# Performance work log

Hardware: AMD Instinct MI355X
Metric: run time of the kernel (lower is better)

## Reference

```python
import jax, jax.numpy as jnp
import numpy as np

B, T, C = 4, 2048, 1024
H = 16
D = C // H  # 64


def setup_inputs() -> dict:
    key = jax.random.key(0)
    ks = jax.random.split(key, 3)
    scale = 1.0 / np.sqrt(C)
    return {
        "x": jax.random.normal(ks[0], (B, T, C), dtype=jnp.float32),
        "W_attn": jax.random.normal(ks[1], (C, 3 * C), dtype=jnp.float32) * scale,
        "b_attn": jnp.zeros((3 * C,), dtype=jnp.float32),
        "W_proj": jax.random.normal(ks[2], (C, C), dtype=jnp.float32) * scale,
        "b_proj": jnp.zeros((C,), dtype=jnp.float32),
    }


def reference(x, W_attn, b_attn, W_proj, b_proj):
    b, t, c = x.shape
    qkv = x @ W_attn + b_attn                      # [B,T,3C]
    q, k, v = jnp.split(qkv, 3, axis=-1)           # each [B,T,C]
    to_heads = lambda z: z.reshape(b, t, H, D).transpose(0, 2, 1, 3)  # [B,H,T,D]
    q, k, v = to_heads(q), to_heads(k), to_heads(v)
    scores = jnp.einsum("bhtd,bhsd->bhts", q, k) / jnp.sqrt(jnp.float32(D))
    causal = jnp.tril(jnp.ones((t, t), dtype=bool))  # [T,T]
    scores = jnp.where(causal[None, None], scores, jnp.finfo(scores.dtype).min)
    attn = jax.nn.softmax(scores, axis=-1)           # [B,H,T,T]
    out = jnp.einsum("bhts,bhsd->bhtd", attn, v)     # [B,H,T,D]
    out = out.transpose(0, 2, 1, 3).reshape(b, t, c)
    return out @ W_proj + b_proj
```

## Files before the change

### kernel.cpp

```cpp
#include <hip/hip_runtime.h>
#include <hip/hip_bf16.h>

typedef __bf16 bf16_t;
typedef __attribute__((ext_vector_type(8))) __bf16 bf16x8;
typedef __attribute__((ext_vector_type(4))) float f32x4;
typedef __attribute__((ext_vector_type(4))) unsigned short u16x4;
typedef __attribute__((ext_vector_type(4))) unsigned int u32x4;

#define B_DIM 4
#define T_DIM 2048
#define C_DIM 1024
#define H_DIM 16
#define D_DIM 64
#define M_TOK (B_DIM * T_DIM)
#define N_QKV (3 * C_DIM)
#define NT    (T_DIM / 64)
#define KSTR  72
#define CSC   0.18033688011112042f

__device__ __forceinline__ void gload_lds16(const bf16_t* g, bf16_t* l) {
  __builtin_amdgcn_global_load_lds((const __attribute__((address_space(1))) void*)(g),
                                   (__attribute__((address_space(3))) void*)(l), 16, 0, 0);
}

__global__ void cvt_f32_to_bf16(const float* __restrict__ in, bf16_t* __restrict__ out, int n4) {
  int i = blockIdx.x * blockDim.x + threadIdx.x;
  if (i >= n4) return;
  float4 v = ((const float4*)in)[i];
  struct alignas(8) bv4 { bf16_t x, y, z, w; };
  bv4 o;
  o.x = (bf16_t)v.x; o.y = (bf16_t)v.y; o.z = (bf16_t)v.z; o.w = (bf16_t)v.w;
  ((bv4*)out)[i] = o;
}

__global__ void transpose_f32_to_bf16(const float* __restrict__ in, bf16_t* __restrict__ out,
                                      int K, int N) {
  __shared__ float tile[32][33];
  int bx = blockIdx.x * 32;
  int by = blockIdx.y * 32;
  int tx = threadIdx.x, ty = threadIdx.y;
#pragma unroll
  for (int i = 0; i < 32; i += 8)
    tile[ty + i][tx] = in[(size_t)(by + ty + i) * N + bx + tx];
  __syncthreads();
#pragma unroll
  for (int i = 0; i < 32; i += 8)
    out[(size_t)(bx + ty + i) * K + by + tx] = (bf16_t)tile[tx][ty + i];
}

#define BM 128
#define BN 128
#define BK 32

__global__ __launch_bounds__(256, 4)
void gemm_bt_bias(const bf16_t* __restrict__ A, const bf16_t* __restrict__ Bt,
                  const float* __restrict__ bias, bf16_t* __restrict__ Cb,
                  int M, int N, int K) {
  __shared__ alignas(16) bf16_t As[BM * BK];
  __shared__ alignas(16) bf16_t Bs[BN * BK];
  const int tid = threadIdx.x;
  const int lane = tid & 63;
  const int wave = tid >> 6;
  const int wr = (wave >> 1) * 64, wc = (wave & 1) * 64;
  const int quad = lane >> 4, l16 = lane & 15;
  const int row0 = blockIdx.x * BM, col0 = blockIdx.y * BN;

  const int srow = wave * 32 + (lane >> 2);
  const int scol = (lane & 3) * 8;
  const bf16_t* Ag = A + (size_t)(row0 + srow) * K + scol;
  const bf16_t* Bg = Bt + (size_t)(col0 + srow) * K + scol;
  bf16_t* AsW = &As[(wave * 32) * BK];
  bf16_t* BsW = &Bs[(wave * 32) * BK];

  f32x4 acc[4][4];
#pragma unroll
  for (int i = 0; i < 4; ++i)
#pragma unroll
    for (int j = 0; j < 4; ++j)
      acc[i][j] = (f32x4){0.f, 0.f, 0.f, 0.f};

  for (int k0 = 0; k0 < K; k0 += BK) {
    __syncthreads();
    gload_lds16(Ag + k0, AsW);
    gload_lds16(Ag + k0 + (size_t)16 * K, AsW + 16 * BK);
    gload_lds16(Bg + k0, BsW);
    gload_lds16(Bg + k0 + (size_t)16 * K, BsW + 16 * BK);
    __syncthreads();
    bf16x8 af[4], bfr[4];
#pragma unroll
    for (int i = 0; i < 4; ++i)
      af[i] = *(const bf16x8*)&As[(wr + i * 16 + l16) * BK + quad * 8];
#pragma unroll
    for (int j = 0; j < 4; ++j)
      bfr[j] = *(const bf16x8*)&Bs[(wc + j * 16 + l16) * BK + quad * 8];
#pragma unroll
    for (int i = 0; i < 4; ++i)
#pragma unroll
      for (int j = 0; j < 4; ++j)
        acc[i][j] = __builtin_amdgcn_mfma_f32_16x16x32_bf16(af[i], bfr[j], acc[i][j], 0, 0, 0);
  }

#pragma unroll
  for (int i = 0; i < 4; ++i)
#pragma unroll
    for (int j = 0; j < 4; ++j) {
      int col = col0 + wc + j * 16 + l16;
      float bv = bias[col];
#pragma unroll
      for (int r = 0; r < 4; ++r) {
        int row = row0 + wr + i * 16 + quad * 4 + r;
        Cb[(size_t)row * N + col] = (bf16_t)(acc[i][j][r] + bv);
      }
    }
}

__global__ __launch_bounds__(256, 4)
void gemm_bt_bias_n64(const bf16_t* __restrict__ A, const bf16_t* __restrict__ Bt,
                      const float* __restrict__ bias, float* __restrict__ Cf,
                      int M, int N, int K) {
  __shared__ alignas(16) bf16_t As[BM * BK];
  __shared__ alignas(16) bf16_t Bs[64 * BK];
  const int tid = threadIdx.x;
  const int lane = tid & 63;
  const int wave = tid >> 6;
  const int wr = (wave >> 1) * 64, wc = (wave & 1) * 32;
  const int quad = lane >> 4, l16 = lane & 15;
  const int row0 = blockIdx.x * BM, col0 = blockIdx.y * 64;

  const int sr = lane >> 2;
  const int scol = (lane & 3) * 8;
  const bf16_t* Ag = A + (size_t)(row0 + wave * 32 + sr) * K + scol;
  const bf16_t* Bg = Bt + (size_t)(col0 + wave * 16 + sr) * K + scol;
  bf16_t* AsW = &As[(wave * 32) * BK];
  bf16_t* BsW = &Bs[(wave * 16) * BK];

  f32x4 acc[4][2];
#pragma unroll
  for (int i = 0; i < 4; ++i)
#pragma unroll
    for (int j = 0; j < 2; ++j)
      acc[i][j] = (f32x4){0.f, 0.f, 0.f, 0.f};

  for (int k0 = 0; k0 < K; k0 += BK) {
    __syncthreads();
    gload_lds16(Ag + k0, AsW);
    gload_lds16(Ag + k0 + (size_t)16 * K, AsW + 16 * BK);
    gload_lds16(Bg + k0, BsW);
    __syncthreads();
    bf16x8 af[4], bfr[2];
#pragma unroll
    for (int i = 0; i < 4; ++i)
      af[i] = *(const bf16x8*)&As[(wr + i * 16 + l16) * BK + quad * 8];
#pragma unroll
    for (int j = 0; j < 2; ++j)
      bfr[j] = *(const bf16x8*)&Bs[(wc + j * 16 + l16) * BK + quad * 8];
#pragma unroll
    for (int i = 0; i < 4; ++i)
#pragma unroll
      for (int j = 0; j < 2; ++j)
        acc[i][j] = __builtin_amdgcn_mfma_f32_16x16x32_bf16(af[i], bfr[j], acc[i][j], 0, 0, 0);
  }

#pragma unroll
  for (int i = 0; i < 4; ++i)
#pragma unroll
    for (int j = 0; j < 2; ++j) {
      int col = col0 + wc + j * 16 + l16;
      float bv = bias[col];
#pragma unroll
      for (int r = 0; r < 4; ++r) {
        int row = row0 + wr + i * 16 + quad * 4 + r;
        Cf[(size_t)row * N + col] = acc[i][j][r] + bv;
      }
    }
}

__global__ __launch_bounds__(256, 4)
void attn_fwd(const bf16_t* __restrict__ qkv, bf16_t* __restrict__ out) {
  __shared__ alignas(16) bf16_t Ks[64 * KSTR];
  __shared__ alignas(16) bf16_t Vt[64 * KSTR];

  const int tid = threadIdx.x;
  const int lane = tid & 63;
  const int wave = tid >> 6;
  const int quad = lane >> 4, l16 = lane & 15;
  const int qlo = blockIdx.x;
  const int qhi = NT - 1 - qlo;
  const int h = blockIdx.y, b = blockIdx.z;
  const size_t tokBase = (size_t)b * T_DIM;

  const bf16_t* qpl = qkv + (tokBase + qlo * 64 + wave * 16 + l16) * N_QKV + h * D_DIM;
  const bf16_t* qph = qkv + (tokBase + qhi * 64 + wave * 16 + l16) * N_QKV + h * D_DIM;
  bf16x8 ql0 = *(const bf16x8*)(qpl + quad * 8);
  bf16x8 ql1 = *(const bf16x8*)(qpl + 32 + quad * 8);
  bf16x8 qh0 = *(const bf16x8*)(qph + quad * 8);
  bf16x8 qh1 = *(const bf16x8*)(qph + 32 + quad * 8);

  f32x4 ol[4], oh[4];
#pragma unroll
  for (int dt = 0; dt < 4; ++dt) {
    ol[dt] = (f32x4){0.f, 0.f, 0.f, 0.f};
    oh[dt] = (f32x4){0.f, 0.f, 0.f, 0.f};
  }
  float ll = 0.f, lh = 0.f;

  const int tx = tid & 15, ty = tid >> 4;
  const int vswz = ((tx >> 2) & 3) * 8;
  const int vcol = (8 * (ty & 3) + 4 * ((ty >> 2) & 1) + 32 * (ty >> 3)) ^ vswz;
  const f32x4 zero4 = (f32x4){0.f, 0.f, 0.f, 0.f};

  u16x4 kreg[4], vreg[4];
  const bf16_t* kb0 = qkv + (tokBase + ty * 4) * N_QKV + h * D_DIM + C_DIM + tx * 4;
#pragma unroll
  for (int r = 0; r < 4; ++r) kreg[r] = *(const u16x4*)(kb0 + (size_t)r * N_QKV);
#pragma unroll
  for (int r = 0; r < 4; ++r) vreg[r] = *(const u16x4*)(kb0 + (size_t)r * N_QKV + C_DIM);

  for (int t = 0; t <= qhi; ++t) {
    const bool lo = (t <= qlo);
    __syncthreads();
#pragma unroll
    for (int r = 0; r < 4; ++r)
      *(u16x4*)&Ks[(ty * 4 + r) * KSTR + tx * 4] = kreg[r];
#pragma unroll
    for (int i = 0; i < 4; ++i) {
      u16x4 p = (u16x4){vreg[0][i], vreg[1][i], vreg[2][i], vreg[3][i]};
      *(u16x4*)&Vt[(tx * 4 + i) * KSTR + vcol] = p;
    }
    __syncthreads();
    if (t < qhi) {
      const bf16_t* kb = qkv + (tokBase + (t + 1) * 64 + ty * 4) * N_QKV + h * D_DIM + C_DIM + tx * 4;
#pragma unroll
      for (int r = 0; r < 4; ++r) kreg[r] = *(const u16x4*)(kb + (size_t)r * N_QKV);
#pragma unroll
      for (int r = 0; r < 4; ++r) vreg[r] = *(const u16x4*)(kb + (size_t)r * N_QKV + C_DIM);
    }

    f32x4 svl[4], svh[4];
#pragma unroll
    for (int ct = 0; ct < 4; ++ct) {
      bf16x8 kf0 = *(const bf16x8*)&Ks[(ct * 16 + l16) * KSTR + quad * 8];
      bf16x8 kf1 = *(const bf16x8*)&Ks[(ct * 16 + l16) * KSTR + 32 + quad * 8];
      if (lo) {
        svl[ct] = __builtin_amdgcn_mfma_f32_16x16x32_bf16(kf0, ql0, zero4, 0, 0, 0);
        svl[ct] = __builtin_amdgcn_mfma_f32_16x16x32_bf16(kf1, ql1, svl[ct], 0, 0, 0);
      }
      svh[ct] = __builtin_amdgcn_mfma_f32_16x16x32_bf16(kf0, qh0, zero4, 0, 0, 0);
      svh[ct] = __builtin_amdgcn_mfma_f32_16x16x32_bf16(kf1, qh1, svh[ct], 0, 0, 0);
    }
    if (t == qlo) {
      const int qr = wave * 16 + l16;
#pragma unroll
      for (int ct = 0; ct < 4; ++ct)
#pragma unroll
        for (int r = 0; r < 4; ++r)
          if (ct * 16 + quad * 4 + r > qr) svl[ct][r] = -INFINITY;
    }
    if (t == qhi) {
      const int qr = wave * 16 + l16;
#pragma unroll
      for (int ct = 0; ct < 4; ++ct)
#pragma unroll
        for (int r = 0; r < 4; ++r)
          if (ct * 16 + quad * 4 + r > qr) svh[ct][r] = -INFINITY;
    }

    struct alignas(4) bpair { bf16_t lo, hi; };
    bf16x8 pl0, pl1, ph0, ph1;
    if (lo) {
      float rsum = 0.f;
      unsigned int lw[8];
#pragma unroll
      for (int ct = 0; ct < 4; ++ct) {
        float e0 = __builtin_amdgcn_exp2f(svl[ct][0] * CSC);
        float e1 = __builtin_amdgcn_exp2f(svl[ct][1] * CSC);
        float e2 = __builtin_amdgcn_exp2f(svl[ct][2] * CSC);
        float e3 = __builtin_amdgcn_exp2f(svl[ct][3] * CSC);
        rsum += (e0 + e1) + (e2 + e3);
        bpair w0 = {(bf16_t)e0, (bf16_t)e1};
        bpair w1 = {(bf16_t)e2, (bf16_t)e3};
        lw[ct * 2 + 0] = __builtin_bit_cast(unsigned int, w0);
        lw[ct * 2 + 1] = __builtin_bit_cast(unsigned int, w1);
      }
      rsum += __shfl_xor(rsum, 16);
      rsum += __shfl_xor(rsum, 32);
      ll += rsum;
      u32x4 pw0 = (u32x4){lw[0], lw[1], lw[2], lw[3]};
      u32x4 pw1 = (u32x4){lw[4], lw[5], lw[6], lw[7]};
      pl0 = __builtin_bit_cast(bf16x8, pw0);
      pl1 = __builtin_bit_cast(bf16x8, pw1);
    }
    {
      float rsum = 0.f;
      unsigned int lw[8];
#pragma unroll
      for (int ct = 0; ct < 4; ++ct) {
        float e0 = __builtin_amdgcn_exp2f(svh[ct][0] * CSC);
        float e1 = __builtin_amdgcn_exp2f(svh[ct][1] * CSC);
        float e2 = __builtin_amdgcn_exp2f(svh[ct][2] * CSC);
        float e3 = __builtin_amdgcn_exp2f(svh[ct][3] * CSC);
        rsum += (e0 + e1) + (e2 + e3);
        bpair w0 = {(bf16_t)e0, (bf16_t)e1};
        bpair w1 = {(bf16_t)e2, (bf16_t)e3};
        lw[ct * 2 + 0] = __builtin_bit_cast(unsigned int, w0);
        lw[ct * 2 + 1] = __builtin_bit_cast(unsigned int, w1);
      }
      rsum += __shfl_xor(rsum, 16);
      rsum += __shfl_xor(rsum, 32);
      lh += rsum;
      u32x4 pw0 = (u32x4){lw[0], lw[1], lw[2], lw[3]};
      u32x4 pw1 = (u32x4){lw[4], lw[5], lw[6], lw[7]};
      ph0 = __builtin_bit_cast(bf16x8, pw0);
      ph1 = __builtin_bit_cast(bf16x8, pw1);
    }

#pragma unroll
    for (int dt = 0; dt < 4; ++dt) {
      const int vc = (quad * 8) ^ (dt * 8);
      bf16x8 vf0 = *(const bf16x8*)&Vt[(dt * 16 + l16) * KSTR + vc];
      bf16x8 vf1 = *(const bf16x8*)&Vt[(dt * 16 + l16) * KSTR + 32 + vc];
      if (lo) {
        ol[dt] = __builtin_amdgcn_mfma_f32_16x16x32_bf16(vf0, pl0, ol[dt], 0, 0, 0);
        ol[dt] = __builtin_amdgcn_mfma_f32_16x16x32_bf16(vf1, pl1, ol[dt], 0, 0, 0);
      }
      oh[dt] = __builtin_amdgcn_mfma_f32_16x16x32_bf16(vf0, ph0, oh[dt], 0, 0, 0);
      oh[dt] = __builtin_amdgcn_mfma_f32_16x16x32_bf16(vf1, ph1, oh[dt], 0, 0, 0);
    }
  }

  struct alignas(8) bh4 { bf16_t a, b, c, d; };
  {
    float rl = 1.0f / ll;
    bf16_t* op = out + (tokBase + qlo * 64 + wave * 16 + l16) * C_DIM + h * D_DIM;
#pragma unroll
    for (int dt = 0; dt < 4; ++dt) {
      bh4 v = {(bf16_t)(ol[dt][0] * rl), (bf16_t)(ol[dt][1] * rl),
               (bf16_t)(ol[dt][2] * rl), (bf16_t)(ol[dt][3] * rl)};
      *(bh4*)(op + dt * 16 + quad * 4) = v;
    }
  }
  {
    float rl = 1.0f / lh;
    bf16_t* op = out + (tokBase + qhi * 64 + wave * 16 + l16) * C_DIM + h * D_DIM;
#pragma unroll
    for (int dt = 0; dt < 4; ++dt) {
      bh4 v = {(bf16_t)(oh[dt][0] * rl), (bf16_t)(oh[dt][1] * rl),
               (bf16_t)(oh[dt][2] * rl), (bf16_t)(oh[dt][3] * rl)};
      *(bh4*)(op + dt * 16 + quad * 4) = v;
    }
  }
}

extern "C" void kernel_launch(void* const* d_in, const int* in_sizes, int n_in,
                              void* d_out, int out_size, void* d_ws, size_t ws_size,
                              hipStream_t stream) {
  const float* x      = (const float*)d_in[0];
  const float* W_attn = (const float*)d_in[1];
  const float* b_attn = (const float*)d_in[2];
  const float* W_proj = (const float*)d_in[3];
  const float* b_proj = (const float*)d_in[4];
  float* out = (float*)d_out;

  char* ws = (char*)d_ws;
  bf16_t* xb   = (bf16_t*)ws;  ws += (size_t)M_TOK * C_DIM * 2;
  bf16_t* Wat  = (bf16_t*)ws;  ws += (size_t)N_QKV * C_DIM * 2;
  bf16_t* Wpt  = (bf16_t*)ws;  ws += (size_t)C_DIM * C_DIM * 2;
  bf16_t* qkv  = (bf16_t*)ws;  ws += (size_t)M_TOK * N_QKV * 2;
  bf16_t* attn = (bf16_t*)ws;  ws += (size_t)M_TOK * C_DIM * 2;

  {
    int n4 = (M_TOK * C_DIM) / 4;
    cvt_f32_to_bf16<<<n4 / 256, 256, 0, stream>>>(x, xb, n4);
  }
  transpose_f32_to_bf16<<<dim3(N_QKV / 32, C_DIM / 32), dim3(32, 8), 0, stream>>>(W_attn, Wat, C_DIM, N_QKV);
  transpose_f32_to_bf16<<<dim3(C_DIM / 32, C_DIM / 32), dim3(32, 8), 0, stream>>>(W_proj, Wpt, C_DIM, C_DIM);

  gemm_bt_bias<<<dim3(M_TOK / BM, N_QKV / BN), 256, 0, stream>>>(
      xb, Wat, b_attn, qkv, M_TOK, N_QKV, C_DIM);

  attn_fwd<<<dim3(NT / 2, H_DIM, B_DIM), 256, 0, stream>>>(qkv, attn);

  gemm_bt_bias_n64<<<dim3(M_TOK / BM, C_DIM / 64), 256, 0, stream>>>(
      attn, Wpt, b_proj, out, M_TOK, C_DIM, C_DIM);
}
```

Baseline: 273.7 us.

## Double-buffer K/V tiles in LDS and raise wave priority around MFMA blocks

The attention kernel now holds two K and two transposed-V tiles in shared memory. It writes the next tile into the alternate buffer while the current one is consumed, so each iteration needs one barrier instead of two. s_setprio is raised around the QK and PV MFMA sections so waves issuing matrix work get scheduling preference. This doubles LDS use per block (about 36KB), which may reduce occupancy relative to the launch bound of 4 blocks.

```diff
diff --git a/kernel.cpp b/kernel.cpp
--- a/kernel.cpp
+++ b/kernel.cpp
@@ -16,6 +16,7 @@
 #define N_QKV (3 * C_DIM)
 #define NT    (T_DIM / 64)
 #define KSTR  72
+#define TILE_E (64 * KSTR)
 #define CSC   0.18033688011112042f
 
 __device__ __forceinline__ void gload_lds16(const bf16_t* g, bf16_t* l) {
@@ -177,8 +178,8 @@
 
 __global__ __launch_bounds__(256, 4)
 void attn_fwd(const bf16_t* __restrict__ qkv, bf16_t* __restrict__ out) {
-  __shared__ alignas(16) bf16_t Ks[64 * KSTR];
-  __shared__ alignas(16) bf16_t Vt[64 * KSTR];
+  __shared__ alignas(16) bf16_t Ks[2][TILE_E];
+  __shared__ alignas(16) bf16_t Vt[2][TILE_E];
 
   const int tid = threadIdx.x;
   const int lane = tid & 63;
@@ -215,19 +216,20 @@
   for (int r = 0; r < 4; ++r) kreg[r] = *(const u16x4*)(kb0 + (size_t)r * N_QKV);
 #pragma unroll
   for (int r = 0; r < 4; ++r) vreg[r] = *(const u16x4*)(kb0 + (size_t)r * N_QKV + C_DIM);
+#pragma unroll
+  for (int r = 0; r < 4; ++r)
+    *(u16x4*)&Ks[0][(ty * 4 + r) * KSTR + tx * 4] = kreg[r];
+#pragma unroll
+  for (int i = 0; i < 4; ++i) {
+    u16x4 p = (u16x4){vreg[0][i], vreg[1][i], vreg[2][i], vreg[3][i]};
+    *(u16x4*)&Vt[0][(tx * 4 + i) * KSTR + vcol] = p;
+  }
+  __syncthreads();
 
   for (int t = 0; t <= qhi; ++t) {
+    const int cur = t & 1;
     const bool lo = (t <= qlo);
-    __syncthreads();
-#pragma unroll
-    for (int r = 0; r < 4; ++r)
-      *(u16x4*)&Ks[(ty * 4 + r) * KSTR + tx * 4] = kreg[r];
-#pragma unroll
-    for (int i = 0; i < 4; ++i) {
-      u16x4 p = (u16x4){vreg[0][i], vreg[1][i], vreg[2][i], vreg[3][i]};
-      *(u16x4*)&Vt[(tx * 4 + i) * KSTR + vcol] = p;
-    }
-    __syncthreads();
+
     if (t < qhi) {
       const bf16_t* kb = qkv + (tokBase + (t + 1) * 64 + ty * 4) * N_QKV + h * D_DIM + C_DIM + tx * 4;
 #pragma unroll
@@ -237,10 +239,11 @@
     }
 
     f32x4 svl[4], svh[4];
+    __builtin_amdgcn_s_setprio(1);
 #pragma unroll
     for (int ct = 0; ct < 4; ++ct) {
-      bf16x8 kf0 = *(const bf16x8*)&Ks[(ct * 16 + l16) * KSTR + quad * 8];
-      bf16x8 kf1 = *(const bf16x8*)&Ks[(ct * 16 + l16) * KSTR + 32 + quad * 8];
+      bf16x8 kf0 = *(const bf16x8*)&Ks[cur][(ct * 16 + l16) * KSTR + quad * 8];
+      bf16x8 kf1 = *(const bf16x8*)&Ks[cur][(ct * 16 + l16) * KSTR + 32 + quad * 8];
       if (lo) {
         svl[ct] = __builtin_amdgcn_mfma_f32_16x16x32_bf16(kf0, ql0, zero4, 0, 0, 0);
         svl[ct] = __builtin_amdgcn_mfma_f32_16x16x32_bf16(kf1, ql1, svl[ct], 0, 0, 0);
@@ -248,6 +251,7 @@
       svh[ct] = __builtin_amdgcn_mfma_f32_16x16x32_bf16(kf0, qh0, zero4, 0, 0, 0);
       svh[ct] = __builtin_amdgcn_mfma_f32_16x16x32_bf16(kf1, qh1, svh[ct], 0, 0, 0);
     }
+    __builtin_amdgcn_s_setprio(0);
     if (t == qlo) {
       const int qr = wave * 16 + l16;
 #pragma unroll
@@ -314,11 +318,23 @@
       ph1 = __builtin_bit_cast(bf16x8, pw1);
     }
 
+    if (t < qhi) {
+#pragma unroll
+      for (int r = 0; r < 4; ++r)
+        *(u16x4*)&Ks[cur ^ 1][(ty * 4 + r) * KSTR + tx * 4] = kreg[r];
+#pragma unroll
+      for (int i = 0; i < 4; ++i) {
+        u16x4 p = (u16x4){vreg[0][i], vreg[1][i], vreg[2][i], vreg[3][i]};
+        *(u16x4*)&Vt[cur ^ 1][(tx * 4 + i) * KSTR + vcol] = p;
+      }
+    }
+
+    __builtin_amdgcn_s_setprio(1);
 #pragma unroll
     for (int dt = 0; dt < 4; ++dt) {
       const int vc = (quad * 8) ^ (dt * 8);
-      bf16x8 vf0 = *(const bf16x8*)&Vt[(dt * 16 + l16) * KSTR + vc];
-      bf16x8 vf1 = *(const bf16x8*)&Vt[(dt * 16 + l16) * KSTR + 32 + vc];
+      bf16x8 vf0 = *(const bf16x8*)&Vt[cur][(dt * 16 + l16) * KSTR + vc];
+      bf16x8 vf1 = *(const bf16x8*)&Vt[cur][(dt * 16 + l16) * KSTR + 32 + vc];
       if (lo) {
         ol[dt] = __builtin_amdgcn_mfma_f32_16x16x32_bf16(vf0, pl0, ol[dt], 0, 0, 0);
         ol[dt] = __builtin_amdgcn_mfma_f32_16x16x32_bf16(vf1, pl1, ol[dt], 0, 0, 0);
@@ -326,6 +342,9 @@
       oh[dt] = __builtin_amdgcn_mfma_f32_16x16x32_bf16(vf0, ph0, oh[dt], 0, 0, 0);
       oh[dt] = __builtin_amdgcn_mfma_f32_16x16x32_bf16(vf1, ph1, oh[dt], 0, 0, 0);
     }
+    __builtin_amdgcn_s_setprio(0);
+
+    __syncthreads();
   }
 
   struct alignas(8) bh4 { bf16_t a, b, c, d; };
```

After: 272.4 us. Within noise of the previous version (-0.5%).
